# Optimization experiments

Measured on AMD Instinct MI355X. Metric: run time of the kernel, lower is better.

Reference implementation:

```python
import jax, jax.numpy as jnp
import numpy as np

N_NODES = 100000
N_EDGES = 1600000
D_IN, D_H, D_OUT = 128, 128, 40
BN_EPS = 1e-5


def _glorot(k, shape):
    lim = float(np.sqrt(6.0 / (shape[0] + shape[1])))
    return jax.random.uniform(k, shape, jnp.float32, -lim, lim)


def setup_inputs() -> dict:
    key = jax.random.key(0)
    ks = jax.random.split(key, 8)
    return {
        "x": jax.random.normal(ks[0], (N_NODES, D_IN), jnp.float32),
        "edge_index": jax.random.randint(ks[1], (2, N_EDGES), 0, N_NODES, jnp.int32),
        "w1": _glorot(ks[2], (D_IN, D_H)), "r1": _glorot(ks[3], (D_IN, D_H)),
        "b1": jnp.zeros((D_H,), jnp.float32),
        "g1": jnp.ones((D_H,), jnp.float32), "be1": jnp.zeros((D_H,), jnp.float32),
        "w2": _glorot(ks[4], (D_H, D_H)), "r2": _glorot(ks[5], (D_H, D_H)),
        "b2": jnp.zeros((D_H,), jnp.float32),
        "g2": jnp.ones((D_H,), jnp.float32), "be2": jnp.zeros((D_H,), jnp.float32),
        "w3": _glorot(ks[6], (D_H, D_OUT)), "r3": _glorot(ks[7], (D_H, D_OUT)),
        "b3": jnp.zeros((D_OUT,), jnp.float32),
    }


def _sage_conv(x, src, dst, w, r, b, n_nodes):
    # mean aggregation over incoming edges: adj.matmul(x, reduce='mean')
    agg = jax.ops.segment_sum(x[src], dst, num_segments=n_nodes)  # [N, D]
    deg = jax.ops.segment_sum(jnp.ones_like(src, dtype=x.dtype), dst, num_segments=n_nodes)
    mean = agg / jnp.maximum(deg, 1.0)[:, None]
    return mean @ w + x @ r + b


def _batch_norm(h, gamma, beta):
    # training-mode BN over node dim (batch statistics)
    mu = h.mean(axis=0)
    var = h.var(axis=0)
    return (h - mu) * jax.lax.rsqrt(var + BN_EPS) * gamma + beta


def reference(x, edge_index, w1, r1, b1, g1, be1, w2, r2, b2, g2, be2, w3, r3, b3):
    n = x.shape[0]
    src, dst = edge_index[0], edge_index[1]
    h = _sage_conv(x, src, dst, w1, r1, b1, n)
    h = jax.nn.relu(_batch_norm(h, g1, be1))
    h = _sage_conv(h, src, dst, w2, r2, b2, n)
    h = jax.nn.relu(_batch_norm(h, g2, be2))
    h = _sage_conv(h, src, dst, w3, r3, b3, n)
    return jax.nn.log_softmax(h, axis=-1)
```

## Files before the change

### kernel.cpp

```cpp
#include <hip/hip_runtime.h>
#include <cstdint>
#include <cstddef>
#include <math.h>

#define N_NODES 100000
#define N_EDGES 1600000
#define DIM 128
#define DOUT 40
#define BN_EPS 1e-5f

#define NB 250
#define NPB 400
#define BCAP 8192

typedef __attribute__((ext_vector_type(8))) short bf16x8;
typedef __attribute__((ext_vector_type(4))) float f32x4;

__device__ __forceinline__ float bf2f(uint u16shifted) {
    union { uint i; float f; } c; c.i = u16shifted; return c.f;
}
__device__ __forceinline__ ushort f2bf(float f) {
    union { float f; uint i; } c; c.f = f;
    uint i = c.i;
    uint lsb = (i >> 16) & 1u;
    i += 0x7FFFu + lsb;
    return (ushort)(i >> 16);
}
__device__ __forceinline__ uint bnpack(uint u, float s0, float h0, float s1, float h1) {
    float lo = fmaxf(bf2f(u << 16) * s0 + h0, 0.f);
    float hi = fmaxf(bf2f(u & 0xFFFF0000u) * s1 + h1, 0.f);
    return (uint)f2bf(lo) | ((uint)f2bf(hi) << 16);
}

__device__ __forceinline__ void wcat_body(const float* __restrict__ W,
                                          const float* __restrict__ R,
                                          ushort* __restrict__ out, int NW, int blk) {
    int idx = blk * 256 + threadIdx.x;
    int n = idx >> 8, k = idx & 255;
    float v = 0.f;
    if (n < NW) v = (k < 128) ? W[k * NW + n] : R[(k - 128) * NW + n];
    out[idx] = f2bf(v);
}

__global__ __launch_bounds__(256) void k_prep(const float* __restrict__ x,
                                              ushort* __restrict__ Xb,
                                              const float* __restrict__ w1, const float* __restrict__ r1, ushort* __restrict__ Wc1,
                                              const float* __restrict__ w2, const float* __restrict__ r2, ushort* __restrict__ Wc2,
                                              const float* __restrict__ w3, const float* __restrict__ r3, ushort* __restrict__ Wc3) {
    int b = blockIdx.x;
    if (b < 2048) {
        int n4 = N_NODES * DIM / 4;
        int i = b * 256 + threadIdx.x;
        int stride = 2048 * 256;
        for (; i < n4; i += stride) {
            float4 v = reinterpret_cast<const float4*>(x)[i];
            ushort4 o;
            o.x = f2bf(v.x); o.y = f2bf(v.y); o.z = f2bf(v.z); o.w = f2bf(v.w);
            reinterpret_cast<ushort4*>(Xb)[i] = o;
        }
    } else if (b < 2048 + 128) {
        wcat_body(w1, r1, Wc1, 128, b - 2048);
    } else if (b < 2048 + 256) {
        wcat_body(w2, r2, Wc2, 128, b - 2176);
    } else {
        wcat_body(w3, r3, Wc3, DOUT, b - 2304);
    }
}

__global__ __launch_bounds__(256) void k_bucket(const int* __restrict__ ei,
                                                uint* __restrict__ bucketbuf,
                                                int* __restrict__ gcnt) {
    __shared__ int hist[NB];
    __shared__ int base_[NB];
    int tid = threadIdx.x;
    for (int i = tid; i < NB; i += 256) hist[i] = 0;
    __syncthreads();
    const int EPB = N_EDGES / 256;
    int e0 = blockIdx.x * EPB, e1 = e0 + EPB;
    for (int e = e0 + tid; e < e1; e += 256) {
        int d = ei[N_EDGES + e];
        atomicAdd(&hist[d / NPB], 1);
    }
    __syncthreads();
    for (int i = tid; i < NB; i += 256) base_[i] = atomicAdd(&gcnt[i], hist[i]);
    __syncthreads();
    for (int i = tid; i < NB; i += 256) hist[i] = 0;
    __syncthreads();
    for (int e = e0 + tid; e < e1; e += 256) {
        int d = ei[N_EDGES + e];
        int s = ei[e];
        int b = d / NPB;
        int pos = base_[b] + atomicAdd(&hist[b], 1);
        if (pos < BCAP)
            bucketbuf[(size_t)b * BCAP + pos] = ((uint)(d - b * NPB) << 17) | (uint)s;
    }
}

__global__ void k_bscan(const int* __restrict__ gcnt, int* __restrict__ bbase) {
    if (threadIdx.x == 0) {
        int run = 0;
        for (int b = 0; b < NB; b++) { bbase[b] = run; run += gcnt[b]; }
        bbase[NB] = run;
    }
}

__global__ __launch_bounds__(256) void k_csr_build(const int* __restrict__ ei,
                                                   const uint* __restrict__ bucketbuf,
                                                   const int* __restrict__ gcnt,
                                                   const int* __restrict__ bbase,
                                                   int* __restrict__ rowstart,
                                                   int* __restrict__ csr) {
    __shared__ int cnts[NPB + 1];
    __shared__ int lcur[NPB];
    __shared__ int csr_l[BCAP];
    int b = blockIdx.x, tid = threadIdx.x;
    int cnt = gcnt[b];
    int base = bbase[b];
    int lo = b * NPB;
    bool fits = (cnt <= BCAP);
    for (int i = tid; i < NPB; i += 256) cnts[i] = 0;
    __syncthreads();
    if (fits) {
        for (int i = tid; i < cnt; i += 256)
            atomicAdd(&cnts[bucketbuf[(size_t)b * BCAP + i] >> 17], 1);
    } else {
        for (int e = tid; e < N_EDGES; e += 256) {
            int d = ei[N_EDGES + e];
            if (d >= lo && d < lo + NPB) atomicAdd(&cnts[d - lo], 1);
        }
    }
    __syncthreads();
    if (tid == 0) {
        int run = 0;
        for (int i = 0; i < NPB; i++) { int c = cnts[i]; cnts[i] = run; run += c; }
        cnts[NPB] = run;
    }
    __syncthreads();
    for (int i = tid; i < NPB; i += 256) rowstart[lo + i] = base + cnts[i];
    if (b == NB - 1 && tid == 0) rowstart[N_NODES] = base + cnts[NPB];
    for (int i = tid; i < NPB; i += 256) lcur[i] = 0;
    __syncthreads();
    if (fits) {
        for (int i = tid; i < cnt; i += 256) {
            uint p = bucketbuf[(size_t)b * BCAP + i];
            int dl = p >> 17;
            int pos = cnts[dl] + atomicAdd(&lcur[dl], 1);
            csr_l[pos] = (int)(p & 0x1FFFFu);
        }
        __syncthreads();
        for (int i = tid; i < cnt; i += 256) csr[base + i] = csr_l[i];
    } else {
        for (int e = tid; e < N_EDGES; e += 256) {
            int d = ei[N_EDGES + e];
            if (d >= lo && d < lo + NPB) {
                int dl = d - lo;
                int pos = cnts[dl] + atomicAdd(&lcur[dl], 1);
                csr[base + pos] = ei[e];
            }
        }
    }
}

__global__ __launch_bounds__(256) void k_agg_bf(const ushort* __restrict__ cur,
                                                const int* __restrict__ rowstart,
                                                const int* __restrict__ csr,
                                                ushort* __restrict__ out,
                                                const float* __restrict__ stats,
                                                const float* __restrict__ g,
                                                const float* __restrict__ be,
                                                int hasbn) {
    int wid = (blockIdx.x * blockDim.x + threadIdx.x) >> 6;
    int lane = threadIdx.x & 63;
    if (wid >= N_NODES) return;
    int beg = rowstart[wid];
    int end = rowstart[wid + 1];
    int slot = lane >> 4;
    int cg = lane & 15;
    float scv[8], shv[8];
#pragma unroll
    for (int j = 0; j < 8; j++) { scv[j] = 1.f; shv[j] = 0.f; }
    if (hasbn) {
        int c0 = cg * 8;
#pragma unroll
        for (int j = 0; j < 8; j++) {
            int c = c0 + j;
            float mu = stats[c] * (1.0f / N_NODES);
            float var = stats[128 + c] * (1.0f / N_NODES) - mu * mu;
            float sc = g[c] * rsqrtf(var + BN_EPS);
            scv[j] = sc;
            shv[j] = be[c] - mu * sc;
        }
    }
    const uint4* base = reinterpret_cast<const uint4*>(cur);
    float a0 = 0.f, a1 = 0.f, a2 = 0.f, a3 = 0.f, a4 = 0.f, a5 = 0.f, a6 = 0.f, a7 = 0.f;
#pragma unroll 2
    for (int e = beg + slot; e < end; e += 4) {
        int s = csr[e];
        uint4 u = base[(size_t)s * 16 + cg];
        float v0 = bf2f(u.x << 16), v1 = bf2f(u.x & 0xFFFF0000u);
        float v2 = bf2f(u.y << 16), v3 = bf2f(u.y & 0xFFFF0000u);
        float v4 = bf2f(u.z << 16), v5 = bf2f(u.z & 0xFFFF0000u);
        float v6 = bf2f(u.w << 16), v7 = bf2f(u.w & 0xFFFF0000u);
        if (hasbn) {
            v0 = fmaxf(v0 * scv[0] + shv[0], 0.f); v1 = fmaxf(v1 * scv[1] + shv[1], 0.f);
            v2 = fmaxf(v2 * scv[2] + shv[2], 0.f); v3 = fmaxf(v3 * scv[3] + shv[3], 0.f);
            v4 = fmaxf(v4 * scv[4] + shv[4], 0.f); v5 = fmaxf(v5 * scv[5] + shv[5], 0.f);
            v6 = fmaxf(v6 * scv[6] + shv[6], 0.f); v7 = fmaxf(v7 * scv[7] + shv[7], 0.f);
        }
        a0 += v0; a1 += v1; a2 += v2; a3 += v3;
        a4 += v4; a5 += v5; a6 += v6; a7 += v7;
    }
#pragma unroll
    for (int off = 16; off < 64; off <<= 1) {
        a0 += __shfl_xor(a0, off, 64); a1 += __shfl_xor(a1, off, 64);
        a2 += __shfl_xor(a2, off, 64); a3 += __shfl_xor(a3, off, 64);
        a4 += __shfl_xor(a4, off, 64); a5 += __shfl_xor(a5, off, 64);
        a6 += __shfl_xor(a6, off, 64); a7 += __shfl_xor(a7, off, 64);
    }
    if (slot == 0) {
        int deg = end - beg;
        float inv = 1.0f / (float)(deg > 1 ? deg : 1);
        uint4 o;
        o.x = (uint)f2bf(a0 * inv) | ((uint)f2bf(a1 * inv) << 16);
        o.y = (uint)f2bf(a2 * inv) | ((uint)f2bf(a3 * inv) << 16);
        o.z = (uint)f2bf(a4 * inv) | ((uint)f2bf(a5 * inv) << 16);
        o.w = (uint)f2bf(a6 * inv) | ((uint)f2bf(a7 * inv) << 16);
        reinterpret_cast<uint4*>(out)[(size_t)wid * 16 + cg] = o;
    }
}

__global__ __launch_bounds__(256, 2) void k_gemm_mfma(const ushort* __restrict__ Am,
                                                      const ushort* __restrict__ Ac,
                                                      const ushort* __restrict__ Wcat,
                                                      const float* __restrict__ bias,
                                                      const float* __restrict__ stats_in,
                                                      const float* __restrict__ g,
                                                      const float* __restrict__ be,
                                                      int hasbn,
                                                      ushort* __restrict__ out,
                                                      float* __restrict__ stats_out,
                                                      int dostats) {
    __shared__ ushort A2[2][128][136];
    __shared__ float scS[128], shS[128];
    __shared__ float lsum[128], lsumsq[128];
    int tid = threadIdx.x;
    int wid = tid >> 6, lane = tid & 63;
    int wr = wid >> 1, wc = wid & 1;
    int l15 = lane & 15, lhi = lane >> 4;
    int row0 = blockIdx.x * 128;

    if (tid < 128) {
        if (hasbn) {
            float mu = stats_in[tid] * (1.0f / N_NODES);
            float var = stats_in[128 + tid] * (1.0f / N_NODES) - mu * mu;
            float sc = g[tid] * rsqrtf(var + BN_EPS);
            scS[tid] = sc;
            shS[tid] = be[tid] - mu * sc;
        }
        lsum[tid] = 0.f;
        lsumsq[tid] = 0.f;
    }
    __syncthreads();

    for (int h = 0; h < 2; ++h) {
        const ushort* Asrc = h ? Ac : Am;
        bool doBN = (h == 1) && hasbn;
#pragma unroll
        for (int i = 0; i < 8; ++i) {
            int idx = i * 256 + tid;
            int row = idx >> 4, q = idx & 15;
            int gr = row0 + row;
            uint4 v = {0, 0, 0, 0};
            if (gr < N_NODES)
                v = *reinterpret_cast<const uint4*>(Asrc + (size_t)gr * 128 + q * 8);
            if (doBN) {
                int cc = q * 8;
                v.x = bnpack(v.x, scS[cc + 0], shS[cc + 0], scS[cc + 1], shS[cc + 1]);
                v.y = bnpack(v.y, scS[cc + 2], shS[cc + 2], scS[cc + 3], shS[cc + 3]);
                v.z = bnpack(v.z, scS[cc + 4], shS[cc + 4], scS[cc + 5], shS[cc + 5]);
                v.w = bnpack(v.w, scS[cc + 6], shS[cc + 6], scS[cc + 7], shS[cc + 7]);
            }
            *reinterpret_cast<uint4*>(&A2[h][row][q * 8]) = v;
        }
    }
    __syncthreads();

    f32x4 acc[4][4];
#pragma unroll
    for (int m = 0; m < 4; m++)
#pragma unroll
        for (int n = 0; n < 4; n++) acc[m][n] = (f32x4){0.f, 0.f, 0.f, 0.f};

#pragma unroll
    for (int ks = 0; ks < 8; ++ks) {
        int kg = ks * 32;
        int half = kg >> 7;
        int ka = (kg & 127) + lhi * 8;
        bf16x8 a[4], b[4];
#pragma unroll
        for (int m = 0; m < 4; m++)
            a[m] = *reinterpret_cast<bf16x8*>(&A2[half][wr * 64 + m * 16 + l15][ka]);
#pragma unroll
        for (int n = 0; n < 4; n++)
            b[n] = *reinterpret_cast<const bf16x8*>(Wcat + (wc * 64 + n * 16 + l15) * 256 + kg + lhi * 8);
#pragma unroll
        for (int m = 0; m < 4; m++)
#pragma unroll
            for (int n = 0; n < 4; n++)
                acc[m][n] = __builtin_amdgcn_mfma_f32_16x16x32_bf16(a[m], b[n], acc[m][n], 0, 0, 0);
    }
    float ps[4] = {0.f, 0.f, 0.f, 0.f}, ps2[4] = {0.f, 0.f, 0.f, 0.f};
#pragma unroll
    for (int m = 0; m < 4; m++) {
        int rbase = row0 + wr * 64 + m * 16 + lhi * 4;
#pragma unroll
        for (int n = 0; n < 4; n++) {
            int col = wc * 64 + n * 16 + l15;
            float bv = bias[col];
#pragma unroll
            for (int j = 0; j < 4; j++) {
                int gr = rbase + j;
                if (gr < N_NODES) {
                    float v = acc[m][n][j] + bv;
                    out[(size_t)gr * 128 + col] = f2bf(v);
                    ps[n] += v;
                    ps2[n] += v * v;
                }
            }
        }
    }
    if (dostats) {
#pragma unroll
        for (int n = 0; n < 4; n++) {
            ps[n] += __shfl_xor(ps[n], 16, 64);
            ps2[n] += __shfl_xor(ps2[n], 16, 64);
            ps[n] += __shfl_xor(ps[n], 32, 64);
            ps2[n] += __shfl_xor(ps2[n], 32, 64);
        }
        if (lhi == 0) {
#pragma unroll
            for (int n = 0; n < 4; n++) {
                int col = wc * 64 + n * 16 + l15;
                atomicAdd(&lsum[col], ps[n]);
                atomicAdd(&lsumsq[col], ps2[n]);
            }
        }
        __syncthreads();
        if (tid < 128) {
            atomicAdd(&stats_out[tid], lsum[tid]);
            atomicAdd(&stats_out[128 + tid], lsumsq[tid]);
        }
    }
}

__global__ __launch_bounds__(256, 2) void k_gemm40_mfma(const ushort* __restrict__ Am,
                                                        const ushort* __restrict__ Ac,
                                                        const ushort* __restrict__ Wcat,
                                                        const float* __restrict__ bias,
                                                        const float* __restrict__ stats_in,
                                                        const float* __restrict__ g,
                                                        const float* __restrict__ be,
                                                        float* __restrict__ out) {
    __shared__ ushort A2[2][128][136];
    __shared__ float scS[128], shS[128];
    int tid = threadIdx.x;
    int w = tid >> 6, lane = tid & 63;
    int l15 = lane & 15, lhi = lane >> 4;
    int row0 = blockIdx.x * 128;

    if (tid < 128) {
        float mu = stats_in[tid] * (1.0f / N_NODES);
        float var = stats_in[128 + tid] * (1.0f / N_NODES) - mu * mu;
        float sc = g[tid] * rsqrtf(var + BN_EPS);
        scS[tid] = sc;
        shS[tid] = be[tid] - mu * sc;
    }
    __syncthreads();

    for (int h = 0; h < 2; ++h) {
        const ushort* Asrc = h ? Ac : Am;
#pragma unroll
        for (int i = 0; i < 8; ++i) {
            int idx = i * 256 + tid;
            int row = idx >> 4, q = idx & 15;
            int gr = row0 + row;
            uint4 v = {0, 0, 0, 0};
            if (gr < N_NODES)
                v = *reinterpret_cast<const uint4*>(Asrc + (size_t)gr * 128 + q * 8);
            if (h == 1) {
                int cc = q * 8;
                v.x = bnpack(v.x, scS[cc + 0], shS[cc + 0], scS[cc + 1], shS[cc + 1]);
                v.y = bnpack(v.y, scS[cc + 2], shS[cc + 2], scS[cc + 3], shS[cc + 3]);
                v.z = bnpack(v.z, scS[cc + 4], shS[cc + 4], scS[cc + 5], shS[cc + 5]);
                v.w = bnpack(v.w, scS[cc + 6], shS[cc + 6], scS[cc + 7], shS[cc + 7]);
            }
            *reinterpret_cast<uint4*>(&A2[h][row][q * 8]) = v;
        }
    }
    __syncthreads();

    f32x4 acc[2][3];
#pragma unroll
    for (int m = 0; m < 2; m++)
#pragma unroll
        for (int n = 0; n < 3; n++) acc[m][n] = (f32x4){0.f, 0.f, 0.f, 0.f};

#pragma unroll
    for (int ks = 0; ks < 8; ++ks) {
        int kg = ks * 32;
        int half = kg >> 7;
        int ka = (kg & 127) + lhi * 8;
        bf16x8 a[2], b[3];
#pragma unroll
        for (int m = 0; m < 2; m++)
            a[m] = *reinterpret_cast<bf16x8*>(&A2[half][w * 32 + m * 16 + l15][ka]);
#pragma unroll
        for (int n = 0; n < 3; n++)
            b[n] = *reinterpret_cast<const bf16x8*>(Wcat + (n * 16 + l15) * 256 + kg + lhi * 8);
#pragma unroll
        for (int m = 0; m < 2; m++)
#pragma unroll
            for (int n = 0; n < 3; n++)
                acc[m][n] = __builtin_amdgcn_mfma_f32_16x16x32_bf16(a[m], b[n], acc[m][n], 0, 0, 0);
    }
    float b0 = bias[l15];
    float b1 = bias[16 + l15];
    float b2 = (l15 < 8) ? bias[32 + l15] : 0.f;
#pragma unroll
    for (int m = 0; m < 2; m++) {
#pragma unroll
        for (int j = 0; j < 4; j++) {
            int grow = row0 + w * 32 + m * 16 + lhi * 4 + j;
            float v0 = acc[m][0][j] + b0;
            float v1 = acc[m][1][j] + b1;
            float v2 = (l15 < 8) ? (acc[m][2][j] + b2) : -INFINITY;
            float mx = fmaxf(fmaxf(v0, v1), v2);
#pragma unroll
            for (int off = 1; off < 16; off <<= 1) mx = fmaxf(mx, __shfl_xor(mx, off, 64));
            float s = expf(v0 - mx) + expf(v1 - mx) + ((l15 < 8) ? expf(v2 - mx) : 0.f);
#pragma unroll
            for (int off = 1; off < 16; off <<= 1) s += __shfl_xor(s, off, 64);
            float lg = mx + logf(s);
            if (grow < N_NODES) {
                out[(size_t)grow * DOUT + l15] = v0 - lg;
                out[(size_t)grow * DOUT + 16 + l15] = v1 - lg;
                if (l15 < 8) out[(size_t)grow * DOUT + 32 + l15] = v2 - lg;
            }
        }
    }
}

extern "C" void kernel_launch(void* const* d_in, const int* in_sizes, int n_in,
                              void* d_out, int out_size, void* d_ws, size_t ws_size,
                              hipStream_t stream) {
    const float* x = (const float*)d_in[0];
    const int* ei = (const int*)d_in[1];
    const float* w1 = (const float*)d_in[2];
    const float* r1 = (const float*)d_in[3];
    const float* b1 = (const float*)d_in[4];
    const float* g1 = (const float*)d_in[5];
    const float* be1 = (const float*)d_in[6];
    const float* w2 = (const float*)d_in[7];
    const float* r2 = (const float*)d_in[8];
    const float* b2 = (const float*)d_in[9];
    const float* g2 = (const float*)d_in[10];
    const float* be2 = (const float*)d_in[11];
    const float* w3 = (const float*)d_in[12];
    const float* r3 = (const float*)d_in[13];
    const float* b3 = (const float*)d_in[14];
    float* out = (float*)d_out;

    const size_t NF = (size_t)N_NODES * DIM;
    ushort* Xb = (ushort*)d_ws;
    ushort* Ab = Xb + NF;
    ushort* Bb = Ab + NF;
    ushort* Wc1 = Bb + NF;
    ushort* Wc2 = Wc1 + 128 * 256;
    ushort* Wc3 = Wc2 + 128 * 256;
    uint* bucketbuf = (uint*)(Wc3 + 48 * 256);
    int* gcnt = (int*)(bucketbuf + (size_t)NB * BCAP);
    float* statsA = (float*)(gcnt + NB);
    float* statsB = statsA + 256;
    int* bbase = (int*)(statsB + 256);
    int* rowstart = bbase + NB + 1;
    int* csr = rowstart + (N_NODES + 1);
    size_t needed = (size_t)((char*)(csr + N_EDGES) - (char*)d_ws);
    if (ws_size < needed) return;

    const int AGG_BLOCKS = N_NODES / 4;
    const int GEMM_BLOCKS = (N_NODES + 127) / 128;

    k_prep<<<2352, 256, 0, stream>>>(x, Xb, w1, r1, Wc1, w2, r2, Wc2, w3, r3, Wc3);
    hipMemsetAsync(gcnt, 0, (NB + 512) * sizeof(int), stream);

    k_bucket<<<256, 256, 0, stream>>>(ei, bucketbuf, gcnt);
    k_bscan<<<1, 64, 0, stream>>>(gcnt, bbase);
    k_csr_build<<<NB, 256, 0, stream>>>(ei, bucketbuf, gcnt, bbase, rowstart, csr);

    k_agg_bf<<<AGG_BLOCKS, 256, 0, stream>>>(Xb, rowstart, csr, Ab, nullptr, nullptr, nullptr, 0);
    k_gemm_mfma<<<GEMM_BLOCKS, 256, 0, stream>>>(Ab, Xb, Wc1, b1, nullptr, nullptr, nullptr, 0,
                                                 Ab, statsA, 1);

    k_agg_bf<<<AGG_BLOCKS, 256, 0, stream>>>(Ab, rowstart, csr, Bb, statsA, g1, be1, 1);
    k_gemm_mfma<<<GEMM_BLOCKS, 256, 0, stream>>>(Bb, Ab, Wc2, b2, statsA, g1, be1, 1,
                                                 Bb, statsB, 1);

    k_agg_bf<<<AGG_BLOCKS, 256, 0, stream>>>(Bb, rowstart, csr, Ab, statsB, g2, be2, 1);
    k_gemm40_mfma<<<GEMM_BLOCKS, 256, 0, stream>>>(Ab, Bb, Wc3, b3, statsB, g2, be2, out);
}
```

Measured before the change: 439.0 us.

## Fuse bucketing into prep kernel, drop scan kernel, pre-swizzle weights for MFMA

Merges the edge-bucketing kernel into the prep kernel as extra blocks, and removes the single-thread bucket scan by having each CSR-build block sum the preceding bucket counts itself. This cuts two kernel launches and a serial scan from the preprocessing chain. Concatenated weights are also stored in a fragment-major layout so each lane's MFMA B operand is a contiguous 16-byte load. In exchange, each CSR block does redundant prefix work, and the last rowstart entry is hardcoded to N_EDGES, which assumes every edge was bucketed.

```diff
diff --git a/kernel.cpp b/kernel.cpp
--- a/kernel.cpp
+++ b/kernel.cpp
@@ -39,18 +39,24 @@
     int n = idx >> 8, k = idx & 255;
     float v = 0.f;
     if (n < NW) v = (k < 128) ? W[k * NW + n] : R[(k - 128) * NW + n];
-    out[idx] = f2bf(v);
+    int fc = n >> 4, l15 = n & 15;
+    int ks = k >> 5, lhi = (k & 31) >> 3, j = k & 7;
+    out[(fc * 8 + ks) * 512 + (lhi * 16 + l15) * 8 + j] = f2bf(v);
 }
 
 __global__ __launch_bounds__(256) void k_prep(const float* __restrict__ x,
                                               ushort* __restrict__ Xb,
                                               const float* __restrict__ w1, const float* __restrict__ r1, ushort* __restrict__ Wc1,
                                               const float* __restrict__ w2, const float* __restrict__ r2, ushort* __restrict__ Wc2,
-                                              const float* __restrict__ w3, const float* __restrict__ r3, ushort* __restrict__ Wc3) {
+                                              const float* __restrict__ w3, const float* __restrict__ r3, ushort* __restrict__ Wc3,
+                                              const int* __restrict__ ei,
+                                              uint* __restrict__ bucketbuf,
+                                              int* __restrict__ gcnt) {
     int b = blockIdx.x;
+    int tid = threadIdx.x;
     if (b < 2048) {
         int n4 = N_NODES * DIM / 4;
-        int i = b * 256 + threadIdx.x;
+        int i = b * 256 + tid;
         int stride = 2048 * 256;
         for (; i < n4; i += stride) {
             float4 v = reinterpret_cast<const float4*>(x)[i];
@@ -62,64 +68,55 @@
         wcat_body(w1, r1, Wc1, 128, b - 2048);
     } else if (b < 2048 + 256) {
         wcat_body(w2, r2, Wc2, 128, b - 2176);
+    } else if (b < 2048 + 304) {
+        wcat_body(w3, r3, Wc3, DOUT, b - 2304);
     } else {
-        wcat_body(w3, r3, Wc3, DOUT, b - 2304);
-    }
-}
-
-__global__ __launch_bounds__(256) void k_bucket(const int* __restrict__ ei,
-                                                uint* __restrict__ bucketbuf,
-                                                int* __restrict__ gcnt) {
-    __shared__ int hist[NB];
-    __shared__ int base_[NB];
-    int tid = threadIdx.x;
-    for (int i = tid; i < NB; i += 256) hist[i] = 0;
-    __syncthreads();
-    const int EPB = N_EDGES / 256;
-    int e0 = blockIdx.x * EPB, e1 = e0 + EPB;
-    for (int e = e0 + tid; e < e1; e += 256) {
-        int d = ei[N_EDGES + e];
-        atomicAdd(&hist[d / NPB], 1);
-    }
-    __syncthreads();
-    for (int i = tid; i < NB; i += 256) base_[i] = atomicAdd(&gcnt[i], hist[i]);
-    __syncthreads();
-    for (int i = tid; i < NB; i += 256) hist[i] = 0;
-    __syncthreads();
-    for (int e = e0 + tid; e < e1; e += 256) {
-        int d = ei[N_EDGES + e];
-        int s = ei[e];
-        int b = d / NPB;
-        int pos = base_[b] + atomicAdd(&hist[b], 1);
-        if (pos < BCAP)
-            bucketbuf[(size_t)b * BCAP + pos] = ((uint)(d - b * NPB) << 17) | (uint)s;
-    }
-}
-
-__global__ void k_bscan(const int* __restrict__ gcnt, int* __restrict__ bbase) {
-    if (threadIdx.x == 0) {
-        int run = 0;
-        for (int b = 0; b < NB; b++) { bbase[b] = run; run += gcnt[b]; }
-        bbase[NB] = run;
+        __shared__ int hist[NB];
+        __shared__ int base_[NB];
+        int blk = b - 2352;
+        for (int i = tid; i < NB; i += 256) hist[i] = 0;
+        __syncthreads();
+        const int EPB = N_EDGES / 256;
+        int e0 = blk * EPB, e1 = e0 + EPB;
+        for (int e = e0 + tid; e < e1; e += 256) {
+            int d = ei[N_EDGES + e];
+            atomicAdd(&hist[d / NPB], 1);
+        }
+        __syncthreads();
+        for (int i = tid; i < NB; i += 256) base_[i] = atomicAdd(&gcnt[i], hist[i]);
+        __syncthreads();
+        for (int i = tid; i < NB; i += 256) hist[i] = 0;
+        __syncthreads();
+        for (int e = e0 + tid; e < e1; e += 256) {
+            int d = ei[N_EDGES + e];
+            int s = ei[e];
+            int bk = d / NPB;
+            int pos = base_[bk] + atomicAdd(&hist[bk], 1);
+            if (pos < BCAP)
+                bucketbuf[(size_t)bk * BCAP + pos] = ((uint)(d - bk * NPB) << 17) | (uint)s;
+        }
     }
 }
 
 __global__ __launch_bounds__(256) void k_csr_build(const int* __restrict__ ei,
                                                    const uint* __restrict__ bucketbuf,
                                                    const int* __restrict__ gcnt,
-                                                   const int* __restrict__ bbase,
                                                    int* __restrict__ rowstart,
                                                    int* __restrict__ csr) {
     __shared__ int cnts[NPB + 1];
     __shared__ int lcur[NPB];
     __shared__ int csr_l[BCAP];
+    __shared__ int baseS;
     int b = blockIdx.x, tid = threadIdx.x;
     int cnt = gcnt[b];
-    int base = bbase[b];
     int lo = b * NPB;
+    if (tid == 0) baseS = 0;
+    for (int i = tid; i < NPB; i += 256) cnts[i] = 0;
+    __syncthreads();
+    int part = 0;
+    for (int i = tid; i < b; i += 256) part += gcnt[i];
+    if (part) atomicAdd(&baseS, part);
     bool fits = (cnt <= BCAP);
-    for (int i = tid; i < NPB; i += 256) cnts[i] = 0;
-    __syncthreads();
     if (fits) {
         for (int i = tid; i < cnt; i += 256)
             atomicAdd(&cnts[bucketbuf[(size_t)b * BCAP + i] >> 17], 1);
@@ -130,6 +127,7 @@
         }
     }
     __syncthreads();
+    int base = baseS;
     if (tid == 0) {
         int run = 0;
         for (int i = 0; i < NPB; i++) { int c = cnts[i]; cnts[i] = run; run += c; }
@@ -137,7 +135,7 @@
     }
     __syncthreads();
     for (int i = tid; i < NPB; i += 256) rowstart[lo + i] = base + cnts[i];
-    if (b == NB - 1 && tid == 0) rowstart[N_NODES] = base + cnts[NPB];
+    if (b == NB - 1 && tid == 0) rowstart[N_NODES] = N_EDGES;
     for (int i = tid; i < NPB; i += 256) lcur[i] = 0;
     __syncthreads();
     if (fits) {
@@ -302,7 +300,7 @@
             a[m] = *reinterpret_cast<bf16x8*>(&A2[half][wr * 64 + m * 16 + l15][ka]);
 #pragma unroll
         for (int n = 0; n < 4; n++)
-            b[n] = *reinterpret_cast<const bf16x8*>(Wcat + (wc * 64 + n * 16 + l15) * 256 + kg + lhi * 8);
+            b[n] = *reinterpret_cast<const bf16x8*>(Wcat + ((wc * 4 + n) * 8 + ks) * 512 + lane * 8);
 #pragma unroll
         for (int m = 0; m < 4; m++)
 #pragma unroll
@@ -416,7 +414,7 @@
             a[m] = *reinterpret_cast<bf16x8*>(&A2[half][w * 32 + m * 16 + l15][ka]);
 #pragma unroll
         for (int n = 0; n < 3; n++)
-            b[n] = *reinterpret_cast<const bf16x8*>(Wcat + (n * 16 + l15) * 256 + kg + lhi * 8);
+            b[n] = *reinterpret_cast<const bf16x8*>(Wcat + (n * 8 + ks) * 512 + lane * 8);
 #pragma unroll
         for (int m = 0; m < 2; m++)
 #pragma unroll
@@ -481,8 +479,7 @@
     int* gcnt = (int*)(bucketbuf + (size_t)NB * BCAP);
     float* statsA = (float*)(gcnt + NB);
     float* statsB = statsA + 256;
-    int* bbase = (int*)(statsB + 256);
-    int* rowstart = bbase + NB + 1;
+    int* rowstart = (int*)(statsB + 256);
     int* csr = rowstart + (N_NODES + 1);
     size_t needed = (size_t)((char*)(csr + N_EDGES) - (char*)d_ws);
     if (ws_size < needed) return;
@@ -490,12 +487,10 @@
     const int AGG_BLOCKS = N_NODES / 4;
     const int GEMM_BLOCKS = (N_NODES + 127) / 128;
 
-    k_prep<<<2352, 256, 0, stream>>>(x, Xb, w1, r1, Wc1, w2, r2, Wc2, w3, r3, Wc3);
     hipMemsetAsync(gcnt, 0, (NB + 512) * sizeof(int), stream);
-
-    k_bucket<<<256, 256, 0, stream>>>(ei, bucketbuf, gcnt);
-    k_bscan<<<1, 64, 0, stream>>>(gcnt, bbase);
-    k_csr_build<<<NB, 256, 0, stream>>>(ei, bucketbuf, gcnt, bbase, rowstart, csr);
+    k_prep<<<2608, 256, 0, stream>>>(x, Xb, w1, r1, Wc1, w2, r2, Wc2, w3, r3, Wc3,
+                                     ei, bucketbuf, gcnt);
+    k_csr_build<<<NB, 256, 0, stream>>>(ei, bucketbuf, gcnt, rowstart, csr);
 
     k_agg_bf<<<AGG_BLOCKS, 256, 0, stream>>>(Xb, rowstart, csr, Ab, nullptr, nullptr, nullptr, 0);
     k_gemm_mfma<<<GEMM_BLOCKS, 256, 0, stream>>>(Ab, Xb, Wc1, b1, nullptr, nullptr, nullptr, 0,
```

Result: faster. 422.5 us (-3.8%).
